# Optimization experiments

Measured on AMD Instinct MI355X. Metric: run time of the kernel, lower is better.

## Reference

```python
import jax, jax.numpy as jnp
import numpy as np

BIG = 1e4  # larger than any image dimension; safe in fp32 when squared


def _edt(e):
    # e: [H, W] binary float mask. Exact Euclidean distance transform:
    # distance from each nonzero pixel to the nearest zero pixel
    # (matches cv2.distanceTransform(e, cv2.DIST_L2, maskSize=0)).
    H, W = e.shape
    zero = e == 0
    x = jnp.arange(W, dtype=jnp.float32)[None, :]            # [1, W]
    # 1D pass along rows: distance (in x) to nearest zero in the same row
    last = jax.lax.cummax(jnp.where(zero, x, -BIG), axis=1)              # nearest zero to the left
    nxt = -jax.lax.cummax(jnp.where(zero, -x, -BIG), axis=1, reverse=True)  # nearest zero to the right
    g = jnp.minimum(x - last, nxt - x)                        # [H, W], BIG-ish if row has no zero
    g2 = jnp.minimum(g, BIG) ** 2                             # squared row distance
    # 2D pass along columns: dist2[y, x] = min_r g2[r, x] + (y - r)^2 (exact EDT)
    y = jnp.arange(H, dtype=jnp.float32)
    d2 = (y[:, None] - y[None, :]) ** 2                       # [H, H]
    dist2 = jnp.min(g2[None, :, :] + d2[:, :, None], axis=1)  # [H, W]
    return jnp.sqrt(dist2)


def _min_max_norm(d):
    lo, hi = d.min(), d.max()
    return (d - lo) / (hi - lo + 1e-8)


def _edge_weight(edge):
    # edge: [B, 1, H, W] binary float
    e = edge[:, 0]  # [B, H, W]
    # lax.map keeps peak memory to one [H,H,W] candidate tensor at a time
    w = jax.lax.map(lambda ei: _min_max_norm(_edt(ei)), e)
    return w[:, None]  # [B, 1, H, W]


def setup_inputs() -> dict:
    key = jax.random.key(0)
    k1, k2, k3, k4 = jax.random.split(key, 4)
    shape = (16, 1, 384, 384)
    eps = 1e-4
    pred = jax.random.uniform(k1, shape, jnp.float32, eps, 1.0 - eps)
    pred_edge = jax.random.uniform(k2, shape, jnp.float32, eps, 1.0 - eps)
    label = jax.random.randint(k3, shape, 0, 2).astype(jnp.float32)
    edge = jax.random.randint(k4, shape, 0, 2).astype(jnp.float32)
    return {"pred": pred, "pred_edge": pred_edge, "label": label, "edge": edge}


def reference(pred, pred_edge, label, edge):
    Wm = _edge_weight(edge)  # [B, 1, H, W] in [0, 1]
    label_loss = jnp.mean(
        -(label * jnp.log(pred) + (1.0 - label) * jnp.log(1.0 - pred)) * (1.0 + Wm)
    )
    edge_loss = jnp.mean(
        -(edge * jnp.log(pred_edge) + (1.0 - edge) * jnp.log(1.0 - pred_edge))
    )
    return label_loss + edge_loss
```

## Files before the change

### kernel.cpp

```cpp
#include <hip/hip_runtime.h>

#define NIMG 16
#define H 384
#define W 384
#define NPIX (H*W)
#define NTOT (NIMG*NPIX)
#define FBIG 10000.0f

#define RPB 96
#define NRB (H/RPB)
#define NCT 12
#define EBLOCKS (NCT*NRB*NIMG)
#define NROW (NIMG*H)

__device__ __forceinline__ float bflo(unsigned int w){ return __uint_as_float(w<<16); }
__device__ __forceinline__ float bfhi(unsigned int w){ return __uint_as_float(w & 0xFFFF0000u); }

__device__ __forceinline__ void detect_flag(const unsigned int* lw, int tid,
                                            unsigned int* sflag) {
    if (tid < 64) {
        unsigned int a = 0;
        #pragma unroll
        for (int k = 0; k < 4; ++k) a |= lw[(tid & 63) * 4 + k] & 0xFFFFu;
        unsigned long long b = __ballot(a != 0u);
        if (tid == 0) *sflag = (b != 0ull) ? 1u : 0u;
    }
}

__global__ __launch_bounds__(256) void rowscan_kernel(
        const void* __restrict__ e, const unsigned int* __restrict__ label_u32,
        float* __restrict__ g2, unsigned int* __restrict__ mn,
        unsigned int* __restrict__ mx) {
    __shared__ unsigned int sflag;
    int tid = threadIdx.x;
    if (blockIdx.x == 0 && tid < NIMG) { mn[tid] = 0x7f800000u; mx[tid] = 0u; }
    detect_flag(label_u32, tid, &sflag);
    __syncthreads();
    bool isb = (sflag != 0u);

    int lane = tid & 63;
    int row  = blockIdx.x * 4 + (tid >> 6);

    unsigned long long zm[6];
    if (isb) {
        const unsigned short* er = (const unsigned short*)e + (size_t)row * W;
        #pragma unroll
        for (int t = 0; t < 6; ++t) zm[t] = __ballot(er[t*64 + lane] == 0);
    } else {
        const float* er = (const float*)e + (size_t)row * W;
        #pragma unroll
        for (int t = 0; t < 6; ++t) zm[t] = __ballot(er[t*64 + lane] == 0.0f);
    }

    float* gr = g2 + (size_t)row * W;
    #pragma unroll
    for (int t = 0; t < 6; ++t) {
        int c = t*64 + lane;
        unsigned long long m = zm[t] & ((lane == 63) ? ~0ull : ((1ull << (lane+1)) - 1ull));
        int tt = t;
        while (m == 0ull && tt > 0) m = zm[--tt];
        float dl = m ? (float)(c - (tt*64 + 63 - __builtin_clzll(m)))
                     : ((float)c + FBIG);
        m = zm[t] & ((lane == 0) ? ~0ull : ~((1ull << lane) - 1ull));
        tt = t;
        while (m == 0ull && tt < 5) m = zm[++tt];
        float dr = m ? (float)((tt*64 + __builtin_ctzll(m)) - c)
                     : (FBIG - (float)c);
        float g = fminf(fminf(dl, dr), FBIG);
        gr[c] = g * g;
    }
}

__global__ __launch_bounds__(256) void edt_loss_kernel(
    const float* __restrict__ g2,
    const void* __restrict__ pred, const void* __restrict__ pred_edge,
    const void* __restrict__ label, const void* __restrict__ edge,
    unsigned int* __restrict__ mn, unsigned int* __restrict__ mx,
    float* __restrict__ partials) {

    __shared__ float4 tile[H * 8];
    __shared__ unsigned int sflag;
    __shared__ float cr[4][5];

    int tid = threadIdx.x;
    int img = blockIdx.z;
    int c0  = blockIdx.x * 32;
    int r0  = blockIdx.y * RPB;

    detect_flag((const unsigned int*)label, tid, &sflag);

    const float* g2i = g2 + (size_t)img * NPIX;
    #pragma unroll
    for (int k = 0; k < 12; ++k) {
        int gi = tid + 256 * k;
        int row = gi >> 3, c2 = gi & 7;
        tile[gi] = *(const float4*)(g2i + row * W + c0 + c2 * 4);
    }
    __syncthreads();

    int c2t = tid & 7;
    int rg  = tid >> 3;
    int rb  = r0 + rg;

    float4 best[3];
    float ub = 0.0f;
    #pragma unroll
    for (int i = 0; i < 3; ++i) {
        best[i] = tile[(rb + 32*i) * 8 + c2t];
        ub = fmaxf(ub, fmaxf(fmaxf(best[i].x, best[i].y), fmaxf(best[i].z, best[i].w)));
    }
    #pragma unroll
    for (int off = 1; off < 64; off <<= 1)
        ub = fmaxf(ub, __shfl_xor(ub, off));
    int jcap = (int)ceilf(sqrtf(ub)) + 1;
    if (jcap > H - 1) jcap = H - 1;

    for (int j = 1; j <= jcap; ++j) {
        float jj = (float)(j * j);
        #pragma unroll
        for (int i = 0; i < 3; ++i) {
            int r  = rb + 32*i;
            int ru = r - j; ru = (ru < 0) ? 0 : ru;
            int rd = r + j; rd = (rd > H-1) ? H-1 : rd;
            float4 vu = tile[ru * 8 + c2t];
            float4 vd = tile[rd * 8 + c2t];
            best[i].x = fminf(best[i].x, fminf(vu.x, vd.x) + jj);
            best[i].y = fminf(best[i].y, fminf(vu.y, vd.y) + jj);
            best[i].z = fminf(best[i].z, fminf(vu.z, vd.z) + jj);
            best[i].w = fminf(best[i].w, fminf(vu.w, vd.w) + jj);
        }
    }

    bool isb = (sflag != 0u);
    float sl = 0.0f, sd = 0.0f, se = 0.0f;
    float tmin = 3.0e38f, tmax = 0.0f;
    #pragma unroll
    for (int i = 0; i < 3; ++i) {
        float dv[4];
        dv[0] = sqrtf(best[i].x); dv[1] = sqrtf(best[i].y);
        dv[2] = sqrtf(best[i].z); dv[3] = sqrtf(best[i].w);
        #pragma unroll
        for (int cc = 0; cc < 4; ++cc) {
            tmin = fminf(tmin, dv[cc]);
            tmax = fmaxf(tmax, dv[cc]);
        }
        int r = rb + 32*i;
        size_t base = (size_t)img * NPIX + (size_t)r * W + c0 + c2t * 4;
        float p[4], q[4], lv[4], ev[4];
        if (isb) {
            uint2 up = *(const uint2*)((const unsigned short*)pred      + base);
            uint2 uq = *(const uint2*)((const unsigned short*)pred_edge + base);
            uint2 ul = *(const uint2*)((const unsigned short*)label     + base);
            uint2 ue = *(const uint2*)((const unsigned short*)edge      + base);
            p[0]=bflo(up.x); p[1]=bfhi(up.x); p[2]=bflo(up.y); p[3]=bfhi(up.y);
            q[0]=bflo(uq.x); q[1]=bfhi(uq.x); q[2]=bflo(uq.y); q[3]=bfhi(uq.y);
            lv[0]=bflo(ul.x); lv[1]=bfhi(ul.x); lv[2]=bflo(ul.y); lv[3]=bfhi(ul.y);
            ev[0]=bflo(ue.x); ev[1]=bfhi(ue.x); ev[2]=bflo(ue.y); ev[3]=bfhi(ue.y);
        } else {
            float4 a = *(const float4*)((const float*)pred      + base);
            float4 b = *(const float4*)((const float*)pred_edge + base);
            float4 c = *(const float4*)((const float*)label     + base);
            float4 e = *(const float4*)((const float*)edge      + base);
            p[0]=a.x; p[1]=a.y; p[2]=a.z; p[3]=a.w;
            q[0]=b.x; q[1]=b.y; q[2]=b.z; q[3]=b.w;
            lv[0]=c.x; lv[1]=c.y; lv[2]=c.z; lv[3]=c.w;
            ev[0]=e.x; ev[1]=e.y; ev[2]=e.z; ev[3]=e.w;
        }
        #pragma unroll
        for (int cc = 0; cc < 4; ++cc) {
            float bl = -__logf((lv[cc] != 0.0f) ? p[cc] : 1.0f - p[cc]);
            sl += bl;
            sd = fmaf(bl, dv[cc], sd);
            se += -__logf((ev[cc] != 0.0f) ? q[cc] : 1.0f - q[cc]);
        }
    }

    #pragma unroll
    for (int off = 1; off < 64; off <<= 1) {
        sl += __shfl_xor(sl, off);
        sd += __shfl_xor(sd, off);
        se += __shfl_xor(se, off);
        tmin = fminf(tmin, __shfl_xor(tmin, off));
        tmax = fmaxf(tmax, __shfl_xor(tmax, off));
    }
    int wv = tid >> 6;
    if ((tid & 63) == 0) {
        cr[wv][0] = sl; cr[wv][1] = sd; cr[wv][2] = se;
        cr[wv][3] = tmin; cr[wv][4] = tmax;
    }
    __syncthreads();
    if (tid == 0) {
        float S1 = cr[0][0] + cr[1][0] + cr[2][0] + cr[3][0];
        float S2 = cr[0][1] + cr[1][1] + cr[2][1] + cr[3][1];
        float Se = cr[0][2] + cr[1][2] + cr[2][2] + cr[3][2];
        float Tm = fminf(fminf(cr[0][3], cr[1][3]), fminf(cr[2][3], cr[3][3]));
        float TM = fmaxf(fmaxf(cr[0][4], cr[1][4]), fmaxf(cr[2][4], cr[3][4]));
        int blk = (blockIdx.z * NRB + blockIdx.y) * NCT + blockIdx.x;
        partials[blk*4 + 0] = S1;
        partials[blk*4 + 1] = S2;
        partials[blk*4 + 2] = Se;
        atomicMin(&mn[img], __float_as_uint(Tm));
        atomicMax(&mx[img], __float_as_uint(TM));
    }
}

__global__ void final_kernel(const float* __restrict__ partials,
                             const unsigned int* __restrict__ mn,
                             const unsigned int* __restrict__ mx,
                             unsigned int* __restrict__ out) {
    __shared__ float a1[256], a2[256], a3[256];
    __shared__ float ci[NIMG], sei[NIMG];
    int tid = threadIdx.x;
    int img = tid >> 4, s = tid & 15;
    float S1 = 0.0f, S2 = 0.0f, Se = 0.0f;
    #pragma unroll
    for (int k = 0; k < 3; ++k) {
        const float* pp = partials + (img * 48 + s + 16 * k) * 4;
        S1 += pp[0]; S2 += pp[1]; Se += pp[2];
    }
    a1[tid] = S1; a2[tid] = S2; a3[tid] = Se;
    __syncthreads();
    for (int st = 8; st > 0; st >>= 1) {
        if ((tid & 15) < st) {
            a1[tid] += a1[tid + st]; a2[tid] += a2[tid + st]; a3[tid] += a3[tid + st];
        }
        __syncthreads();
    }
    if ((tid & 15) == 0) {
        float lo = __uint_as_float(mn[img]);
        float hi = __uint_as_float(mx[img]);
        float inv = 1.0f / (hi - lo + 1e-8f);
        ci[img]  = a1[tid] + (a2[tid] - lo * a1[tid]) * inv;
        sei[img] = a3[tid];
    }
    __syncthreads();
    if (tid == 0) {
        float t = 0.0f;
        for (int i = 0; i < NIMG; ++i) t += ci[i] + sei[i];
        float v = t / (float)NTOT;
        unsigned int fv = __float_as_uint(v);
        unsigned int b  = (fv + 0x7FFFu + ((fv >> 16) & 1u)) >> 16;
        out[0] = (fv & 0xFFFF0000u) | (b & 0xFFFFu);
    }
}

extern "C" void kernel_launch(void* const* d_in, const int* in_sizes, int n_in,
                              void* d_out, int out_size, void* d_ws, size_t ws_size,
                              hipStream_t stream) {
    float* ws = (float*)d_ws;
    float* g2 = ws;
    unsigned int* mn = (unsigned int*)(ws + NTOT);
    unsigned int* mx = mn + 16;
    float* partials  = (float*)(mx + 16);

    rowscan_kernel<<<NROW / 4, 256, 0, stream>>>(d_in[3], (const unsigned int*)d_in[2],
                                                 g2, mn, mx);
    edt_loss_kernel<<<dim3(NCT, NRB, NIMG), 256, 0, stream>>>(
        g2, d_in[0], d_in[1], d_in[2], d_in[3], mn, mx, partials);
    final_kernel<<<1, 256, 0, stream>>>(partials, mn, mx, (unsigned int*)d_out);
}
```

Baseline: 31.22 us.

## Store row zero-bitmasks instead of g2 and fuse final reduction via ticket

The first kernel now writes only 6 u64 zero-bitmasks per row instead of the full float g2 array. The EDT kernel loads each image's masks into shared memory and recomputes row distances locally, which cuts global write and read traffic. The separate final reduction kernel is removed: a last-block ticket counter performs the cross-block reduction, saving one launch. The cost is redundant row-distance recomputation in every column tile, extra shared memory that may lower occupancy, and reliance on threadfence/atomic ordering to get the ticket reduction right.

```diff
diff --git a/kernel.cpp b/kernel.cpp
--- a/kernel.cpp
+++ b/kernel.cpp
@@ -1,4 +1,7 @@
 #include <hip/hip_runtime.h>
+
+typedef unsigned long long u64;
+typedef unsigned int u32;
 
 #define NIMG 16
 #define H 384
@@ -6,95 +9,115 @@
 #define NPIX (H*W)
 #define NTOT (NIMG*NPIX)
 #define FBIG 10000.0f
+#define NWR 6
 
 #define RPB 96
-#define NRB (H/RPB)
+#define NRB 4
 #define NCT 12
 #define EBLOCKS (NCT*NRB*NIMG)
 #define NROW (NIMG*H)
 
-__device__ __forceinline__ float bflo(unsigned int w){ return __uint_as_float(w<<16); }
-__device__ __forceinline__ float bfhi(unsigned int w){ return __uint_as_float(w & 0xFFFF0000u); }
-
-__device__ __forceinline__ void detect_flag(const unsigned int* lw, int tid,
-                                            unsigned int* sflag) {
+__device__ __forceinline__ float bflo(u32 w){ return __uint_as_float(w<<16); }
+__device__ __forceinline__ float bfhi(u32 w){ return __uint_as_float(w & 0xFFFF0000u); }
+
+__device__ __forceinline__ void detect_flag(const u32* lw, int tid, u32* sflag) {
     if (tid < 64) {
-        unsigned int a = 0;
-        #pragma unroll
-        for (int k = 0; k < 4; ++k) a |= lw[(tid & 63) * 4 + k] & 0xFFFFu;
-        unsigned long long b = __ballot(a != 0u);
+        u32 a = 0;
+        #pragma unroll
+        for (int k = 0; k < 4; ++k) a |= lw[(tid & 63)*4 + k] & 0xFFFFu;
+        u64 b = __ballot(a != 0u);
         if (tid == 0) *sflag = (b != 0ull) ? 1u : 0u;
     }
 }
 
-__global__ __launch_bounds__(256) void rowscan_kernel(
-        const void* __restrict__ e, const unsigned int* __restrict__ label_u32,
-        float* __restrict__ g2, unsigned int* __restrict__ mn,
-        unsigned int* __restrict__ mx) {
-    __shared__ unsigned int sflag;
+__global__ __launch_bounds__(256) void mask_kernel(
+        const void* __restrict__ e, const u32* __restrict__ label_u32,
+        u64* __restrict__ gmask, u32* __restrict__ mn, u32* __restrict__ mx,
+        u32* __restrict__ ticket) {
+    __shared__ u32 sflag;
     int tid = threadIdx.x;
-    if (blockIdx.x == 0 && tid < NIMG) { mn[tid] = 0x7f800000u; mx[tid] = 0u; }
+    if (blockIdx.x == 0) {
+        if (tid < NIMG) { mn[tid] = 0x7f800000u; mx[tid] = 0u; }
+        if (tid == 64)  *ticket = 0u;
+    }
     detect_flag(label_u32, tid, &sflag);
     __syncthreads();
     bool isb = (sflag != 0u);
-
     int lane = tid & 63;
     int row  = blockIdx.x * 4 + (tid >> 6);
-
-    unsigned long long zm[6];
+    u64 z0,z1,z2,z3,z4,z5;
     if (isb) {
         const unsigned short* er = (const unsigned short*)e + (size_t)row * W;
-        #pragma unroll
-        for (int t = 0; t < 6; ++t) zm[t] = __ballot(er[t*64 + lane] == 0);
+        z0=__ballot(er[      lane]==0); z1=__ballot(er[ 64+lane]==0);
+        z2=__ballot(er[128+lane]==0);   z3=__ballot(er[192+lane]==0);
+        z4=__ballot(er[256+lane]==0);   z5=__ballot(er[320+lane]==0);
     } else {
         const float* er = (const float*)e + (size_t)row * W;
-        #pragma unroll
-        for (int t = 0; t < 6; ++t) zm[t] = __ballot(er[t*64 + lane] == 0.0f);
-    }
-
-    float* gr = g2 + (size_t)row * W;
-    #pragma unroll
-    for (int t = 0; t < 6; ++t) {
-        int c = t*64 + lane;
-        unsigned long long m = zm[t] & ((lane == 63) ? ~0ull : ((1ull << (lane+1)) - 1ull));
-        int tt = t;
-        while (m == 0ull && tt > 0) m = zm[--tt];
-        float dl = m ? (float)(c - (tt*64 + 63 - __builtin_clzll(m)))
-                     : ((float)c + FBIG);
-        m = zm[t] & ((lane == 0) ? ~0ull : ~((1ull << lane) - 1ull));
-        tt = t;
-        while (m == 0ull && tt < 5) m = zm[++tt];
-        float dr = m ? (float)((tt*64 + __builtin_ctzll(m)) - c)
-                     : (FBIG - (float)c);
-        float g = fminf(fminf(dl, dr), FBIG);
-        gr[c] = g * g;
+        z0=__ballot(er[      lane]==0.0f); z1=__ballot(er[ 64+lane]==0.0f);
+        z2=__ballot(er[128+lane]==0.0f);   z3=__ballot(er[192+lane]==0.0f);
+        z4=__ballot(er[256+lane]==0.0f);   z5=__ballot(er[320+lane]==0.0f);
+    }
+    if (lane == 0) {
+        ulonglong2* mp = (ulonglong2*)(gmask + (size_t)row * NWR);
+        mp[0] = make_ulonglong2(z0,z1);
+        mp[1] = make_ulonglong2(z2,z3);
+        mp[2] = make_ulonglong2(z4,z5);
     }
 }
 
 __global__ __launch_bounds__(256) void edt_loss_kernel(
-    const float* __restrict__ g2,
+    const u64* __restrict__ gmask,
     const void* __restrict__ pred, const void* __restrict__ pred_edge,
     const void* __restrict__ label, const void* __restrict__ edge,
-    unsigned int* __restrict__ mn, unsigned int* __restrict__ mx,
-    float* __restrict__ partials) {
+    u32* __restrict__ mn, u32* __restrict__ mx,
+    float* __restrict__ partials, u32* __restrict__ ticket,
+    u32* __restrict__ out) {
 
     __shared__ float4 tile[H * 8];
-    __shared__ unsigned int sflag;
+    __shared__ u64 smask[H * NWR];
+    __shared__ u32 sflag, islast;
     __shared__ float cr[4][5];
+    __shared__ float a1[256], a2[256], a3[256];
+    __shared__ float ci[NIMG], sei[NIMG];
 
     int tid = threadIdx.x;
     int img = blockIdx.z;
     int c0  = blockIdx.x * 32;
     int r0  = blockIdx.y * RPB;
 
-    detect_flag((const unsigned int*)label, tid, &sflag);
-
-    const float* g2i = g2 + (size_t)img * NPIX;
+    detect_flag((const u32*)label, tid, &sflag);
+
+    const u64* gm = gmask + (size_t)img * H * NWR;
+    #pragma unroll
+    for (int k = 0; k < 9; ++k) smask[tid + 256*k] = gm[tid + 256*k];
+    __syncthreads();
+
     #pragma unroll
     for (int k = 0; k < 12; ++k) {
-        int gi = tid + 256 * k;
-        int row = gi >> 3, c2 = gi & 7;
-        tile[gi] = *(const float4*)(g2i + row * W + c0 + c2 * 4);
+        int gi  = tid + 256*k;
+        int row = gi >> 3, ch = gi & 7;
+        const u64* mrow = smask + row * NWR;
+        float4 g4;
+        float* gp = (float*)&g4;
+        #pragma unroll
+        for (int cc = 0; cc < 4; ++cc) {
+            int c  = c0 + ch*4 + cc;
+            int cw = c >> 6, cb = c & 63;
+            u64 w  = mrow[cw];
+            u64 ml = w & ((cb == 63) ? ~0ull : ((1ull << (cb+1)) - 1ull));
+            int tw = cw;
+            while (ml == 0ull && tw > 0) ml = mrow[--tw];
+            float dl = ml ? (float)(c - (tw*64 + 63 - __builtin_clzll(ml)))
+                          : ((float)c + FBIG);
+            u64 mr = w & ((cb == 0) ? ~0ull : ~((1ull << cb) - 1ull));
+            tw = cw;
+            while (mr == 0ull && tw < NWR-1) mr = mrow[++tw];
+            float dr = mr ? (float)((tw*64 + __builtin_ctzll(mr)) - c)
+                          : (FBIG - (float)c);
+            float g = fminf(fminf(dl, dr), FBIG);
+            gp[cc] = g * g;
+        }
+        tile[gi] = g4;
     }
     __syncthreads();
 
@@ -195,67 +218,67 @@
         float Se = cr[0][2] + cr[1][2] + cr[2][2] + cr[3][2];
         float Tm = fminf(fminf(cr[0][3], cr[1][3]), fminf(cr[2][3], cr[3][3]));
         float TM = fmaxf(fmaxf(cr[0][4], cr[1][4]), fmaxf(cr[2][4], cr[3][4]));
-        int blk = (blockIdx.z * NRB + blockIdx.y) * NCT + blockIdx.x;
+        int blk = (img * NRB + blockIdx.y) * NCT + blockIdx.x;
         partials[blk*4 + 0] = S1;
         partials[blk*4 + 1] = S2;
         partials[blk*4 + 2] = Se;
         atomicMin(&mn[img], __float_as_uint(Tm));
         atomicMax(&mx[img], __float_as_uint(TM));
     }
-}
-
-__global__ void final_kernel(const float* __restrict__ partials,
-                             const unsigned int* __restrict__ mn,
-                             const unsigned int* __restrict__ mx,
-                             unsigned int* __restrict__ out) {
-    __shared__ float a1[256], a2[256], a3[256];
-    __shared__ float ci[NIMG], sei[NIMG];
-    int tid = threadIdx.x;
-    int img = tid >> 4, s = tid & 15;
-    float S1 = 0.0f, S2 = 0.0f, Se = 0.0f;
-    #pragma unroll
-    for (int k = 0; k < 3; ++k) {
-        const float* pp = partials + (img * 48 + s + 16 * k) * 4;
-        S1 += pp[0]; S2 += pp[1]; Se += pp[2];
-    }
-    a1[tid] = S1; a2[tid] = S2; a3[tid] = Se;
-    __syncthreads();
-    for (int st = 8; st > 0; st >>= 1) {
-        if ((tid & 15) < st) {
-            a1[tid] += a1[tid + st]; a2[tid] += a2[tid + st]; a3[tid] += a3[tid + st];
-        }
+    __threadfence();
+    if (tid == 0) {
+        u32 t = atomicAdd(ticket, 1u);
+        islast = (t == EBLOCKS - 1) ? 1u : 0u;
+    }
+    __syncthreads();
+    if (islast) {
+        __threadfence();
+        int fimg = tid >> 4, s = tid & 15;
+        float S1 = 0.0f, S2 = 0.0f, Se = 0.0f;
+        #pragma unroll
+        for (int k = 0; k < 3; ++k) {
+            const float* pp = partials + (fimg * 48 + s + 16*k) * 4;
+            S1 += pp[0]; S2 += pp[1]; Se += pp[2];
+        }
+        a1[tid] = S1; a2[tid] = S2; a3[tid] = Se;
         __syncthreads();
-    }
-    if ((tid & 15) == 0) {
-        float lo = __uint_as_float(mn[img]);
-        float hi = __uint_as_float(mx[img]);
-        float inv = 1.0f / (hi - lo + 1e-8f);
-        ci[img]  = a1[tid] + (a2[tid] - lo * a1[tid]) * inv;
-        sei[img] = a3[tid];
-    }
-    __syncthreads();
-    if (tid == 0) {
-        float t = 0.0f;
-        for (int i = 0; i < NIMG; ++i) t += ci[i] + sei[i];
-        float v = t / (float)NTOT;
-        unsigned int fv = __float_as_uint(v);
-        unsigned int b  = (fv + 0x7FFFu + ((fv >> 16) & 1u)) >> 16;
-        out[0] = (fv & 0xFFFF0000u) | (b & 0xFFFFu);
+        for (int st = 8; st > 0; st >>= 1) {
+            if ((tid & 15) < st) {
+                a1[tid] += a1[tid+st]; a2[tid] += a2[tid+st]; a3[tid] += a3[tid+st];
+            }
+            __syncthreads();
+        }
+        if ((tid & 15) == 0) {
+            float lo = __uint_as_float(atomicOr(&mn[fimg], 0u));
+            float hi = __uint_as_float(atomicOr(&mx[fimg], 0u));
+            float inv = 1.0f / (hi - lo + 1e-8f);
+            ci[fimg]  = a1[tid] + (a2[tid] - lo * a1[tid]) * inv;
+            sei[fimg] = a3[tid];
+        }
+        __syncthreads();
+        if (tid == 0) {
+            float t = 0.0f;
+            for (int i = 0; i < NIMG; ++i) t += ci[i] + sei[i];
+            float v = t / (float)NTOT;
+            u32 fv = __float_as_uint(v);
+            u32 b  = (fv + 0x7FFFu + ((fv >> 16) & 1u)) >> 16;
+            out[0] = (fv & 0xFFFF0000u) | (b & 0xFFFFu);
+        }
     }
 }
 
 extern "C" void kernel_launch(void* const* d_in, const int* in_sizes, int n_in,
                               void* d_out, int out_size, void* d_ws, size_t ws_size,
                               hipStream_t stream) {
-    float* ws = (float*)d_ws;
-    float* g2 = ws;
-    unsigned int* mn = (unsigned int*)(ws + NTOT);
-    unsigned int* mx = mn + 16;
-    float* partials  = (float*)(mx + 16);
-
-    rowscan_kernel<<<NROW / 4, 256, 0, stream>>>(d_in[3], (const unsigned int*)d_in[2],
-                                                 g2, mn, mx);
+    u64* gmask = (u64*)d_ws;
+    u32* mn = (u32*)(gmask + (size_t)NROW * NWR);
+    u32* mx = mn + 16;
+    u32* ticket = mx + 16;
+    float* partials = (float*)(ticket + 16);
+
+    mask_kernel<<<NROW / 4, 256, 0, stream>>>(d_in[3], (const u32*)d_in[2],
+                                              gmask, mn, mx, ticket);
     edt_loss_kernel<<<dim3(NCT, NRB, NIMG), 256, 0, stream>>>(
-        g2, d_in[0], d_in[1], d_in[2], d_in[3], mn, mx, partials);
-    final_kernel<<<1, 256, 0, stream>>>(partials, mn, mx, (unsigned int*)d_out);
-}
+        gmask, d_in[0], d_in[1], d_in[2], d_in[3], mn, mx,
+        partials, ticket, (u32*)d_out);
+}
```

Measured after the change: 115.8 us. 271% more time.
